# Optimization experiments

Hardware: AMD Instinct MI355X
Metric: run time of the kernel (lower is better)

## Reference

```python
import jax, jax.numpy as jnp
import numpy as np

N = 50000       # num vertices
E_SEG = 80000   # num hyperedges
NNZ = 400000    # incidence pairs
FIN = 512       # input feature dim
H = 256         # MLP_hidden
C = 40          # num classes
NLAYER = 2      # All_num_layers
ALPHA = 0.5     # restart_alpha


def _w(k, shape):
    return jax.random.normal(k, shape, jnp.float32) * (1.0 / np.sqrt(shape[0]))


def setup_inputs() -> dict:
    key = jax.random.key(0)
    ks = jax.random.split(key, 12)
    return {
        "x": jax.random.normal(ks[0], (N, FIN), jnp.float32),
        "vertex": jax.random.randint(ks[1], (NNZ,), 0, N),
        "edges": jax.random.randint(ks[2], (NNZ,), 0, E_SEG),
        "lin_in_w": _w(ks[3], (FIN, H)), "lin_in_b": jnp.zeros((H,), jnp.float32),
        "w1": _w(ks[4], (H, H)),   "b1": jnp.zeros((H,), jnp.float32),
        "w2": _w(ks[5], (2 * H, H)), "b2": jnp.zeros((H,), jnp.float32),
        "w3": _w(ks[6], (H, H)),   "b3": jnp.zeros((H,), jnp.float32),
        "cls_w1": _w(ks[7], (H, H)), "cls_b1": jnp.zeros((H,), jnp.float32),
        "cls_w2": _w(ks[8], (H, C)), "cls_b2": jnp.zeros((C,), jnp.float32),
    }


def reference(x, vertex, edges, lin_in_w, lin_in_b, w1, b1, w2, b2, w3, b3,
              cls_w1, cls_b1, cls_w2, cls_b2):
    # input projection (dropout is identity at p=0)
    x = jax.nn.relu(x @ lin_in_w + lin_in_b)           # [N, H]
    x0 = x
    for _ in range(NLAYER):  # same conv weights reused each layer
        # W1 (1-layer MLP = Linear), gather to incidences
        xve = (x @ w1 + b1)[vertex]                    # [NNZ, H]
        # scatter-add to hyperedges
        xe = jax.ops.segment_sum(xve, edges, num_segments=E_SEG)  # [E, H]
        # gather back, concat with vertex feats, W2 (Linear on 2H)
        xev = jnp.concatenate([x[vertex], xe[edges]], axis=-1) @ w2 + b2  # [NNZ, H]
        # scatter-add to vertices
        xv = jax.ops.segment_sum(xev, vertex, num_segments=N)     # [N, H]
        # restart connection + W (Linear) + outer activation
        x = (1.0 - ALPHA) * xv + ALPHA * x0
        x = jax.nn.relu(x @ w3 + b3)
    # classifier MLP (2 layers: Linear -> relu -> Linear)
    h = jax.nn.relu(x @ cls_w1 + cls_b1)
    return h @ cls_w2 + cls_b2                          # [N, C]
```

## Files before the change

### kernel.cpp

```cpp
#include <hip/hip_runtime.h>
#include <hip/hip_bf16.h>
#include <cstdint>
#include <cstddef>

#define HD   256
#define NV   50000
#define NE   80000
#define NNZC 400000
#define FINC 512
#define NCLS 40

using bf16 = __hip_bfloat16;

typedef short bf16x8v __attribute__((ext_vector_type(8)));
typedef float f32x4   __attribute__((ext_vector_type(4)));
typedef unsigned short u16x8 __attribute__((ext_vector_type(8)));

#define NCH_E ((NE + 1023) / 1024)
#define NCH_V ((NV + 1023) / 1024)
#define NBM_V ((NV + 127) / 128)

__device__ __forceinline__ float b2f(unsigned short u) {
    union { unsigned int i; float f; } c; c.i = ((unsigned int)u) << 16; return c.f;
}
__device__ __forceinline__ unsigned short f2b(float f) {
    union { float f; unsigned int i; } c; c.f = f;
    return (unsigned short)((c.i + 0x7FFFu + ((c.i >> 16) & 1u)) >> 16);
}
__device__ __forceinline__ float4 load4f(const bf16* p) {
    ushort4 u = *reinterpret_cast<const ushort4*>(p);
    return make_float4(b2f(u.x), b2f(u.y), b2f(u.z), b2f(u.w));
}
__device__ __forceinline__ void store4(bf16* p, float4 v) {
    ushort4 u; u.x = f2b(v.x); u.y = f2b(v.y); u.z = f2b(v.z); u.w = f2b(v.w);
    *reinterpret_cast<ushort4*>(p) = u;
}

__device__ __forceinline__ void gl_lds16(const bf16* g, short* l) {
    __builtin_amdgcn_global_load_lds(
        (const __attribute__((address_space(1))) unsigned int*)g,
        (__attribute__((address_space(3))) unsigned int*)l,
        16, 0, 0);
}

__global__ __launch_bounds__(256)
void fill_prep_k(unsigned int* __restrict__ fillp, long long filln,
                 const float* __restrict__ lin_w, const float* __restrict__ w1,
                 const float* __restrict__ w2, const float* __restrict__ w3,
                 const float* __restrict__ cw1, const float* __restrict__ cw2,
                 const float* __restrict__ b2,
                 unsigned short* __restrict__ lin_wt, unsigned short* __restrict__ w1_nb,
                 unsigned short* __restrict__ w2a_nb, unsigned short* __restrict__ w2b_nb,
                 unsigned short* __restrict__ w3t, unsigned short* __restrict__ cw1t,
                 unsigned short* __restrict__ cw2t, float* __restrict__ b2w3)
{
    if (blockIdx.x < 128) {
        long long i = (long long)blockIdx.x * 256 + threadIdx.x;
        for (; i < filln; i += 128 * 256) fillp[i] = 0u;
        return;
    }
    int idx = (blockIdx.x - 128) * 256 + threadIdx.x;
    if (idx < 131072) { int n = idx >> 9, k = idx & 511; lin_wt[idx] = f2b(lin_w[k * 256 + n]); return; }
    idx -= 131072;
    if (idx < 65536) { w1_nb[idx] = f2b(w1[idx]); return; }
    idx -= 65536;
    if (idx < 65536) { w2a_nb[idx] = f2b(w2[idx]); return; }
    idx -= 65536;
    if (idx < 65536) { w2b_nb[idx] = f2b(w2[65536 + idx]); return; }
    idx -= 65536;
    if (idx < 65536) { int n = idx >> 8, k = idx & 255; w3t[idx] = f2b(w3[k * 256 + n]); return; }
    idx -= 65536;
    if (idx < 65536) { int n = idx >> 8, k = idx & 255; cw1t[idx] = f2b(cw1[k * 256 + n]); return; }
    idx -= 65536;
    if (idx < 12288) { int n = idx >> 8, k = idx & 255; cw2t[idx] = f2b((n < NCLS) ? cw2[k * NCLS + n] : 0.f); return; }
    idx -= 12288;
    if (idx < 256) {
        float s = 0.f;
        for (int k = 0; k < 256; ++k) s += b2[k] * w3[k * 256 + idx];
        b2w3[idx] = s;
    }
}

__global__ __launch_bounds__(256)
void hist_k(const int* __restrict__ vertex, const int* __restrict__ edges,
            int* __restrict__ cnt_v, int* __restrict__ cnt_e, int nnz)
{
    int i = blockIdx.x * 256 + threadIdx.x;
    if (i < nnz) {
        atomicAdd(&cnt_v[vertex[i]], 1);
        atomicAdd(&cnt_e[edges[i]], 1);
    }
}

__global__ __launch_bounds__(256)
void scan_part2_k(const int* __restrict__ cnt_e, int* __restrict__ off_e, int* __restrict__ part_e,
                  const int* __restrict__ cnt_v, int* __restrict__ off_v, int* __restrict__ part_v)
{
    const int* cnt; int* off; int* part; int n;
    if (blockIdx.y == 0) { cnt = cnt_e; off = off_e; part = part_e; n = NE; }
    else                 { cnt = cnt_v; off = off_v; part = part_v; n = NV; }
    int base = blockIdx.x * 1024;
    if (base >= n) return;
    __shared__ int s[256];
    int idx = base + threadIdx.x * 4;
    int v[4], sum = 0;
    #pragma unroll
    for (int j = 0; j < 4; ++j) { v[j] = (idx + j < n) ? cnt[idx + j] : 0; sum += v[j]; }
    s[threadIdx.x] = sum;
    __syncthreads();
    #pragma unroll
    for (int d = 1; d < 256; d <<= 1) {
        int t = (threadIdx.x >= d) ? s[threadIdx.x - d] : 0;
        __syncthreads();
        s[threadIdx.x] += t;
        __syncthreads();
    }
    int excl = s[threadIdx.x] - sum;
    #pragma unroll
    for (int j = 0; j < 4; ++j) {
        if (idx + j < n) off[idx + j] = excl;
        excl += v[j];
    }
    if (threadIdx.x == 255) part[blockIdx.x] = s[255];
}

__global__ __launch_bounds__(256)
void scan_top2_k(int* __restrict__ part_e, int* __restrict__ end_e,
                 int* __restrict__ part_v, int* __restrict__ end_v)
{
    int* part; int* endp; int nch;
    if (blockIdx.x == 0) { part = part_e; endp = end_e; nch = NCH_E; }
    else                 { part = part_v; endp = end_v; nch = NCH_V; }
    __shared__ int s[256];
    int v = (threadIdx.x < nch) ? part[threadIdx.x] : 0;
    s[threadIdx.x] = v;
    __syncthreads();
    #pragma unroll
    for (int d = 1; d < 256; d <<= 1) {
        int t = (threadIdx.x >= d) ? s[threadIdx.x - d] : 0;
        __syncthreads();
        s[threadIdx.x] += t;
        __syncthreads();
    }
    if (threadIdx.x < nch) part[threadIdx.x] = s[threadIdx.x] - v;
    if (threadIdx.x == 255) *endp = s[255];
}

__global__ __launch_bounds__(256)
void scan_addcur2_k(int* __restrict__ off_e, const int* __restrict__ part_e, int* __restrict__ cur_e,
                    int* __restrict__ off_v, const int* __restrict__ part_v, int* __restrict__ cur_v)
{
    int n; int* off; const int* part; int* cur;
    if (blockIdx.y == 0) { n = NE; off = off_e; part = part_e; cur = cur_e; }
    else                 { n = NV; off = off_v; part = part_v; cur = cur_v; }
    int i = blockIdx.x * 256 + threadIdx.x;
    if (i < n) { int o = off[i] + part[i >> 10]; off[i] = o; cur[i] = o; }
}

__global__ __launch_bounds__(256)
void csr_fill_k(const int* __restrict__ vertex, const int* __restrict__ edges,
                int* __restrict__ cur_e, int* __restrict__ cur_v,
                int* __restrict__ adj_e, int* __restrict__ adj_v, int nnz)
{
    int i = blockIdx.x * 256 + threadIdx.x;
    if (i >= nnz) return;
    int v = vertex[i], e = edges[i];
    adj_e[atomicAdd(&cur_e[e], 1)] = v;
    adj_v[atomicAdd(&cur_v[v], 1)] = e;
}

__global__ __launch_bounds__(256)
void dege2_k(const int* __restrict__ cnt_e, const int* __restrict__ adj_v,
             const int* __restrict__ off_v, int* __restrict__ dege2, int n)
{
    int v = blockIdx.x * 256 + threadIdx.x;
    if (v >= n) return;
    int s = 0;
    for (int j = off_v[v]; j < off_v[v + 1]; ++j) s += cnt_e[adj_v[j]];
    dege2[v] = s;
}

__global__ __launch_bounds__(256)
void b1w23_k(const float* __restrict__ b1, const unsigned short* __restrict__ W23bt,
             float* __restrict__ o)
{
    int n = threadIdx.x;
    float s = 0.f;
    for (int k = 0; k < 256; ++k) s += b1[k] * b2f(W23bt[n * 256 + k]);
    o[n] = s;
}

template<int EPI, bool AF32>
__global__ __launch_bounds__(256)
void mgemm_k(const void* __restrict__ Agv, const bf16* __restrict__ Bt,
             const float* __restrict__ bias, const float* __restrict__ bias2,
             const int* __restrict__ deg, const int* __restrict__ dege2,
             const bf16* __restrict__ Sb, const bf16* __restrict__ z0b,
             const float* __restrict__ b2w3v, const float* __restrict__ b1w23v,
             bf16* __restrict__ Cg, bf16* __restrict__ Cg2, bf16* __restrict__ Cg3,
             int M, int K, int Nc)
{
    const int nbn = Nc >> 7;
    const int nbm = (M + 127) >> 7;
    const int p   = blockIdx.x;
    const int xcd = p & 7;
    const int q   = p >> 3;
    const int cblk = q % nbn;
    const int rblk = q / nbn;
    const int rb   = rblk * 8 + xcd;
    if (rb >= nbm) return;
    const int bn = cblk * 128;
    const int bm = rb * 128;

    __shared__ __align__(16) short As[2][128 * 64];
    __shared__ __align__(16) short Bs[2][128 * 64];

    const int t  = threadIdx.x;
    const int wv = t >> 6, l = t & 63;
    const int wr = wv >> 1, wc = wv & 1;
    const int l15 = l & 15;

    u16x8 sv8[8], zv8[8];
    float bv[4], bw[4], bb1[4];
    if (EPI == 4) {
        const unsigned short* Sp = (const unsigned short*)Sb + ((size_t)(rb * 2 + cblk) * 256 + t) * 64;
        const unsigned short* Zp = (const unsigned short*)z0b + ((size_t)(rb * 2 + cblk) * 256 + t) * 64;
        #pragma unroll
        for (int j = 0; j < 8; ++j) {
            sv8[j] = *reinterpret_cast<const u16x8*>(Sp + j * 8);
            zv8[j] = *reinterpret_cast<const u16x8*>(Zp + j * 8);
        }
        #pragma unroll
        for (int n = 0; n < 4; ++n) {
            int col = bn + wc * 64 + n * 16 + l15;
            bv[n]  = bias[col];
            bw[n]  = b2w3v[col];
            bb1[n] = b1w23v[col];
        }
    }

    f32x4 acc[4][4];
    #pragma unroll
    for (int m = 0; m < 4; ++m)
        #pragma unroll
        for (int n = 0; n < 4; ++n)
            acc[m][n] = (f32x4){0.f, 0.f, 0.f, 0.f};

    const int brow8   = l >> 3;
    const int bcol_sw = (((l & 7) ^ (l >> 3)) * 8);

    auto stage = [&](int buf, int k0) {
        if constexpr (AF32) {
            const float* Af = (const float*)Agv;
            #pragma unroll
            for (int pi = 0; pi < 4; ++pi) {
                int idx8 = pi * 256 + t;
                int row  = idx8 >> 3;
                int cg   = (idx8 & 7) * 8;
                int ga = bm + row; if (ga >= M) ga = M - 1;
                const float* src = Af + (size_t)ga * K + k0 + cg;
                f32x4 u = *reinterpret_cast<const f32x4*>(src);
                f32x4 v = *reinterpret_cast<const f32x4*>(src + 4);
                bf16x8v o;
                o[0] = (short)f2b(u[0]); o[1] = (short)f2b(u[1]);
                o[2] = (short)f2b(u[2]); o[3] = (short)f2b(u[3]);
                o[4] = (short)f2b(v[0]); o[5] = (short)f2b(v[1]);
                o[6] = (short)f2b(v[2]); o[7] = (short)f2b(v[3]);
                *reinterpret_cast<bf16x8v*>(&As[buf][row * 64 + (cg ^ ((row & 7) * 8))]) = o;
            }
        } else {
            const bf16* Ab = (const bf16*)Agv;
            #pragma unroll
            for (int i = 0; i < 4; ++i) {
                int c = wv * 4 + i;
                int row = c * 8 + brow8;
                int ga = bm + row; if (ga >= M) ga = M - 1;
                gl_lds16(Ab + (size_t)ga * K + k0 + bcol_sw, &As[buf][c * 512]);
            }
        }
        #pragma unroll
        for (int i = 0; i < 4; ++i) {
            int c = wv * 4 + i;
            int row = c * 8 + brow8;
            gl_lds16(Bt + (size_t)(bn + row) * K + k0 + bcol_sw, &Bs[buf][c * 512]);
        }
    };

    stage(0, 0);
    __syncthreads();
    const int nk = K >> 6;
    for (int kst = 0; kst < nk; ++kst) {
        int curb = kst & 1;
        if (kst + 1 < nk) stage(curb ^ 1, (kst + 1) * 64);
        #pragma unroll
        for (int ks = 0; ks < 2; ++ks) {
            bf16x8v a[4], b[4];
            const int kb = ks * 64 + (l >> 4) * 16;
            #pragma unroll
            for (int m = 0; m < 4; ++m) {
                int r = wr * 64 + m * 16 + l15;
                a[m] = *reinterpret_cast<const bf16x8v*>(
                           (const char*)&As[curb][0] + r * 128 + (kb ^ ((r & 7) << 4)));
            }
            #pragma unroll
            for (int n = 0; n < 4; ++n) {
                int r = wc * 64 + n * 16 + l15;
                b[n] = *reinterpret_cast<const bf16x8v*>(
                           (const char*)&Bs[curb][0] + r * 128 + (kb ^ ((r & 7) << 4)));
            }
            #pragma unroll
            for (int m = 0; m < 4; ++m)
                #pragma unroll
                for (int n = 0; n < 4; ++n)
                    acc[m][n] = __builtin_amdgcn_mfma_f32_16x16x32_bf16(a[m], b[n], acc[m][n], 0, 0, 0);
        }
        __syncthreads();
    }

    if (EPI == 5) {
        int oi = bn >> 8;
        bf16* CC = (oi == 0) ? Cg : Cg2;
        int c2 = (bn >> 7) & 1;
        unsigned short* P = (unsigned short*)CC + ((size_t)(rb * 2 + c2) * 256 + t) * 64;
        #pragma unroll
        for (int m = 0; m < 4; ++m) {
            u16x8 o0, o1;
            #pragma unroll
            for (int n = 0; n < 2; ++n)
                #pragma unroll
                for (int i = 0; i < 4; ++i) {
                    o0[n * 4 + i] = f2b(acc[m][n][i]);
                    o1[n * 4 + i] = f2b(acc[m][n + 2][i]);
                }
            *reinterpret_cast<u16x8*>(P + m * 16)     = o0;
            *reinterpret_cast<u16x8*>(P + m * 16 + 8) = o1;
        }
    } else if (EPI == 4) {
        #pragma unroll
        for (int m = 0; m < 4; ++m) {
            #pragma unroll
            for (int i = 0; i < 4; ++i) {
                int row = bm + wr * 64 + m * 16 + (l >> 4) * 4 + i;
                if (row >= M) continue;
                float d   = (float)deg[row];
                float de2 = (float)dege2[row];
                size_t base = (size_t)row * Nc + bn + wc * 64 + l15;
                #pragma unroll
                for (int n = 0; n < 4; ++n) {
                    int e = m * 16 + n * 4 + i;
                    float sv = b2f(sv8[e >> 3][e & 7]);
                    float zv = b2f(zv8[e >> 3][e & 7]);
                    float v = 0.5f * (d * (sv + bw[n]) + acc[m][n][i] + de2 * bb1[n])
                              + 0.5f * zv + bv[n];
                    v = fmaxf(v, 0.f);
                    reinterpret_cast<unsigned short*>(Cg)[base + (size_t)n * 16] = f2b(v);
                }
            }
        }
    } else if (EPI == 3) {
        int oi = bn >> 8;
        bf16* CC = (oi == 0) ? Cg : (oi == 1) ? Cg2 : Cg3;
        const float* bb = (oi == 0) ? bias : (oi == 1) ? bias2 : nullptr;
        int cb = bn & 255;
        float bvv[4];
        #pragma unroll
        for (int n = 0; n < 4; ++n)
            bvv[n] = bb ? bb[cb + wc * 64 + n * 16 + l15] : 0.f;
        #pragma unroll
        for (int m = 0; m < 4; ++m) {
            #pragma unroll
            for (int i = 0; i < 4; ++i) {
                int row = bm + wr * 64 + m * 16 + (l >> 4) * 4 + i;
                if (row >= M) continue;
                size_t base = (size_t)row * 256 + cb + wc * 64 + l15;
                #pragma unroll
                for (int n = 0; n < 4; ++n)
                    reinterpret_cast<unsigned short*>(CC)[base + n * 16] = f2b(acc[m][n][i] + bvv[n]);
            }
        }
    } else {
        float bvv[4];
        #pragma unroll
        for (int n = 0; n < 4; ++n)
            bvv[n] = bias ? bias[bn + wc * 64 + n * 16 + l15] : 0.f;
        #pragma unroll
        for (int m = 0; m < 4; ++m) {
            #pragma unroll
            for (int i = 0; i < 4; ++i) {
                int row = bm + wr * 64 + m * 16 + (l >> 4) * 4 + i;
                if (row >= M) continue;
                size_t base = (size_t)row * Nc + bn + wc * 64 + l15;
                #pragma unroll
                for (int n = 0; n < 4; ++n) {
                    float v = acc[m][n][i] + bvv[n];
                    if (EPI == 1) v = fmaxf(v, 0.f);
                    reinterpret_cast<unsigned short*>(Cg)[base + n * 16] = f2b(v);
                }
            }
        }
    }
}

__global__ __launch_bounds__(256)
void gather_sum_k(const bf16* __restrict__ src, const int* __restrict__ adj,
                  const int* __restrict__ off, bf16* __restrict__ dst, int nseg)
{
    int seg = blockIdx.x * 4 + (threadIdx.x >> 6);
    if (seg >= nseg) return;
    int lane = threadIdx.x & 63;
    int s0 = off[seg], s1 = off[seg + 1];
    float4 acc = make_float4(0.f, 0.f, 0.f, 0.f);
    int j = s0;
    for (; j + 4 <= s1; j += 4) {
        int r0 = adj[j], r1 = adj[j + 1], r2 = adj[j + 2], r3 = adj[j + 3];
        float4 v0 = load4f(src + (size_t)r0 * HD + lane * 4);
        float4 v1 = load4f(src + (size_t)r1 * HD + lane * 4);
        float4 v2 = load4f(src + (size_t)r2 * HD + lane * 4);
        float4 v3 = load4f(src + (size_t)r3 * HD + lane * 4);
        acc.x += (v0.x + v1.x) + (v2.x + v3.x);
        acc.y += (v0.y + v1.y) + (v2.y + v3.y);
        acc.z += (v0.z + v1.z) + (v2.z + v3.z);
        acc.w += (v0.w + v1.w) + (v2.w + v3.w);
    }
    for (; j < s1; ++j) {
        float4 v = load4f(src + (size_t)adj[j] * HD + lane * 4);
        acc.x += v.x; acc.y += v.y; acc.z += v.z; acc.w += v.w;
    }
    store4(dst + (size_t)seg * HD + lane * 4, acc);
}

__global__ __launch_bounds__(256)
void cls_mfma_k(const bf16* __restrict__ Hm, const bf16* __restrict__ Wt,
                const float* __restrict__ bias, float* __restrict__ out, int M)
{
    const int wv = threadIdx.x >> 6, l = threadIdx.x & 63;
    const int l15 = l & 15;
    const int r0 = blockIdx.x * 64 + wv * 16;
    f32x4 acc[3];
    #pragma unroll
    for (int n = 0; n < 3; ++n) acc[n] = (f32x4){0.f, 0.f, 0.f, 0.f};

    int arow = r0 + l15; if (arow >= M) arow = M - 1;
    const int ko = (l >> 4) * 8;
    for (int kk = 0; kk < HD; kk += 32) {
        bf16x8v a = *reinterpret_cast<const bf16x8v*>(Hm + (size_t)arow * HD + kk + ko);
        #pragma unroll
        for (int n = 0; n < 3; ++n) {
            bf16x8v b = *reinterpret_cast<const bf16x8v*>(Wt + (size_t)(n * 16 + l15) * HD + kk + ko);
            acc[n] = __builtin_amdgcn_mfma_f32_16x16x32_bf16(a, b, acc[n], 0, 0, 0);
        }
    }
    #pragma unroll
    for (int n = 0; n < 3; ++n) {
        int col = n * 16 + l15;
        if (col >= NCLS) continue;
        float bv = bias[col];
        #pragma unroll
        for (int i = 0; i < 4; ++i) {
            int row = r0 + (l >> 4) * 4 + i;
            if (row < M) out[(size_t)row * NCLS + col] = acc[n][i] + bv;
        }
    }
}

static inline int xcd_grid(int M, int Nc)
{
    int nbm = (M + 127) >> 7;
    int nbn = Nc >> 7;
    return nbn * (((nbm + 7) / 8) * 8);
}

extern "C" void kernel_launch(void* const* d_in, const int* in_sizes, int n_in,
                              void* d_out, int out_size, void* d_ws, size_t ws_size,
                              hipStream_t stream)
{
    const float* x_in   = (const float*)d_in[0];
    const int*   vertex = (const int*)d_in[1];
    const int*   edges  = (const int*)d_in[2];
    const float* lin_w  = (const float*)d_in[3];
    const float* lin_b  = (const float*)d_in[4];
    const float* w1     = (const float*)d_in[5];
    const float* b1     = (const float*)d_in[6];
    const float* w2     = (const float*)d_in[7];
    const float* b2     = (const float*)d_in[8];
    const float* w3     = (const float*)d_in[9];
    const float* b3     = (const float*)d_in[10];
    const float* cw1    = (const float*)d_in[11];
    const float* cb1    = (const float*)d_in[12];
    const float* cw2    = (const float*)d_in[13];
    const float* cb2    = (const float*)d_in[14];
    float* out = (float*)d_out;
    (void)in_sizes; (void)n_in; (void)out_size; (void)ws_size;

    char* ws = (char*)d_ws;
    const size_t nvhd = (size_t)NV * HD, nehd = (size_t)NE * HD;
    const size_t permsz = (size_t)(NBM_V + 1) * 2 * 256 * 64;
    size_t off = 0;
    auto alloc = [&](size_t bytes) { char* p = ws + off; off += (bytes + 255) & ~(size_t)255; return p; };
    bf16* x0 = (bf16*)alloc(nvhd * 2);
    bf16* xA = (bf16*)alloc(nvhd * 2);
    bf16* E1 = (bf16*)alloc(nehd * 2);
    bf16* E2 = (bf16*)alloc(nehd * 2);
    bf16* S  = (bf16*)alloc(permsz * 2);
    bf16* z0 = (bf16*)alloc(permsz * 2);
    unsigned short* W23at  = (unsigned short*)alloc(2 * 256 * 256 * 2);
    unsigned short* w3t    = W23at + 65536;
    unsigned short* W23bt  = (unsigned short*)alloc(256 * 256 * 2);
    unsigned short* W123bt = (unsigned short*)alloc(256 * 256 * 2);
    unsigned short* w2ab   = (unsigned short*)alloc(512 * 256 * 2);
    unsigned short* w2a_nb = w2ab;
    unsigned short* w2b_nb = w2ab + 256 * 256;
    unsigned short* w1_nb  = (unsigned short*)alloc(256 * 256 * 2);
    unsigned short* lin_wt = (unsigned short*)alloc(256 * 512 * 2);
    unsigned short* cw1t   = (unsigned short*)alloc(256 * 256 * 2);
    unsigned short* cw2t   = (unsigned short*)alloc(48 * 256 * 2);
    float* b2w3  = (float*)alloc(256 * 4);
    float* b1w23 = (float*)alloc(256 * 4);
    int* cnt_e = (int*)alloc(NE * 4);
    int* cnt_v = (int*)alloc(NV * 4);
    int* dege2 = (int*)alloc(NV * 4);
    int* off_e = (int*)alloc((NE + 1) * 4);
    int* off_v = (int*)alloc((NV + 1) * 4);
    int* cur_e = (int*)alloc(NE * 4);
    int* cur_v = (int*)alloc(NV * 4);
    int* part_e = (int*)alloc(256 * 4);
    int* part_v = (int*)alloc(256 * 4);
    int* adj_e = (int*)alloc((size_t)NNZC * 4);
    int* adj_v = (int*)alloc((size_t)NNZC * 4);

    dim3 blk(256);

    fill_prep_k<<<128 + 1841, blk, 0, stream>>>((unsigned int*)cnt_e, NE + NV,
        lin_w, w1, w2, w3, cw1, cw2, b2,
        lin_wt, w1_nb, w2a_nb, w2b_nb, w3t, cw1t, cw2t, b2w3);
    hist_k<<<(NNZC + 255) / 256, blk, 0, stream>>>(vertex, edges, cnt_v, cnt_e, NNZC);
    scan_part2_k<<<dim3(NCH_E, 2), blk, 0, stream>>>(cnt_e, off_e, part_e, cnt_v, off_v, part_v);
    scan_top2_k<<<2, blk, 0, stream>>>(part_e, off_e + NE, part_v, off_v + NV);
    scan_addcur2_k<<<dim3((NE + 255) / 256, 2), blk, 0, stream>>>(off_e, part_e, cur_e,
                                                                  off_v, part_v, cur_v);
    csr_fill_k<<<(NNZC + 255) / 256, blk, 0, stream>>>(vertex, edges, cur_e, cur_v, adj_e, adj_v, NNZC);
    dege2_k<<<(NV + 255) / 256, blk, 0, stream>>>(cnt_e, adj_v, off_v, dege2, NV);

    mgemm_k<3, false><<<xcd_grid(256, 512), blk, 0, stream>>>((const bf16*)w3t, (const bf16*)w2ab,
        nullptr, nullptr, nullptr, nullptr, nullptr, nullptr, nullptr, nullptr,
        (bf16*)W23at, (bf16*)W23bt, nullptr, 256, 256, 512);
    mgemm_k<0, false><<<xcd_grid(256, 256), blk, 0, stream>>>((const bf16*)W23bt, (const bf16*)w1_nb,
        nullptr, nullptr, nullptr, nullptr, nullptr, nullptr, nullptr, nullptr,
        (bf16*)W123bt, nullptr, nullptr, 256, 256, 256);
    b1w23_k<<<1, blk, 0, stream>>>(b1, W23bt, b1w23);

    mgemm_k<1, true><<<xcd_grid(NV, 256), blk, 0, stream>>>(x_in, (const bf16*)lin_wt,
        lin_b, nullptr, nullptr, nullptr, nullptr, nullptr, nullptr, nullptr,
        x0, nullptr, nullptr, NV, FINC, HD);

    const bf16* cur = x0;
    for (int layer = 0; layer < 2; ++layer) {
        if (layer == 0) {
            mgemm_k<5, false><<<xcd_grid(NV, 512), blk, 0, stream>>>(cur, (const bf16*)W23at,
                nullptr, nullptr, nullptr, nullptr, nullptr, nullptr, nullptr, nullptr,
                S, z0, nullptr, NV, HD, 512);
        } else {
            mgemm_k<5, false><<<xcd_grid(NV, 256), blk, 0, stream>>>(cur, (const bf16*)W23at,
                nullptr, nullptr, nullptr, nullptr, nullptr, nullptr, nullptr, nullptr,
                S, nullptr, nullptr, NV, HD, HD);
        }
        gather_sum_k<<<(NE + 3) / 4, blk, 0, stream>>>(cur, adj_e, off_e, E2, NE);
        gather_sum_k<<<(NV + 3) / 4, blk, 0, stream>>>(E2, adj_v, off_v, E1, NV);
        mgemm_k<4, false><<<xcd_grid(NV, 256), blk, 0, stream>>>(E1, (const bf16*)W123bt,
            b3, nullptr, cnt_v, dege2, S, z0, b2w3, b1w23,
            xA, nullptr, nullptr, NV, HD, HD);
        cur = xA;
    }

    mgemm_k<1, false><<<xcd_grid(NV, 256), blk, 0, stream>>>(xA, (const bf16*)cw1t,
        cb1, nullptr, nullptr, nullptr, nullptr, nullptr, nullptr, nullptr,
        E1, nullptr, nullptr, NV, HD, HD);
    cls_mfma_k<<<(NV + 63) / 64, blk, 0, stream>>>(E1, (const bf16*)cw2t, cb2, out, NV);
}
```

Measured before the change: 481.2 us.

## Load A fragments directly from global, stage full 256-wide B slab in LDS

The GEMM kernel stops staging A tiles through double-buffered LDS. Each lane now reads its A fragments straight from global memory, converting from fp32 when needed, while B is loaded into LDS as a whole 128x256 slab once per 256-wide K chunk. This drops the A shared-memory round trip and most per-step barriers. In exchange, A reads are uncoalesced, redundant across the two column waves, and no longer overlap with compute. The larger 64KB B buffer may also reduce occupancy.

```diff
diff --git a/kernel.cpp b/kernel.cpp
--- a/kernel.cpp
+++ b/kernel.cpp
@@ -212,8 +212,7 @@
     const int bn = cblk * 128;
     const int bm = rb * 128;
 
-    __shared__ __align__(16) short As[2][128 * 64];
-    __shared__ __align__(16) short Bs[2][128 * 64];
+    __shared__ __align__(16) short Bs[128 * 256];
 
     const int t  = threadIdx.x;
     const int wv = t >> 6, l = t & 63;
@@ -248,65 +247,60 @@
 
     const int brow8   = l >> 3;
     const int bcol_sw = (((l & 7) ^ (l >> 3)) * 8);
-
-    auto stage = [&](int buf, int k0) {
-        if constexpr (AF32) {
-            const float* Af = (const float*)Agv;
-            #pragma unroll
-            for (int pi = 0; pi < 4; ++pi) {
-                int idx8 = pi * 256 + t;
-                int row  = idx8 >> 3;
-                int cg   = (idx8 & 7) * 8;
-                int ga = bm + row; if (ga >= M) ga = M - 1;
-                const float* src = Af + (size_t)ga * K + k0 + cg;
-                f32x4 u = *reinterpret_cast<const f32x4*>(src);
-                f32x4 v = *reinterpret_cast<const f32x4*>(src + 4);
-                bf16x8v o;
-                o[0] = (short)f2b(u[0]); o[1] = (short)f2b(u[1]);
-                o[2] = (short)f2b(u[2]); o[3] = (short)f2b(u[3]);
-                o[4] = (short)f2b(v[0]); o[5] = (short)f2b(v[1]);
-                o[6] = (short)f2b(v[2]); o[7] = (short)f2b(v[3]);
-                *reinterpret_cast<bf16x8v*>(&As[buf][row * 64 + (cg ^ ((row & 7) * 8))]) = o;
-            }
-        } else {
-            const bf16* Ab = (const bf16*)Agv;
+    const int ko8     = (l >> 4) * 8;
+
+    size_t arow[4];
+    #pragma unroll
+    for (int m = 0; m < 4; ++m) {
+        int ga = bm + wr * 64 + m * 16 + l15; if (ga >= M) ga = M - 1;
+        arow[m] = (size_t)ga * K;
+    }
+
+    for (int kh = 0; kh < K; kh += 256) {
+        if (kh > 0) __syncthreads();
+        #pragma unroll
+        for (int s = 0; s < 4; ++s) {
             #pragma unroll
             for (int i = 0; i < 4; ++i) {
                 int c = wv * 4 + i;
                 int row = c * 8 + brow8;
-                int ga = bm + row; if (ga >= M) ga = M - 1;
-                gl_lds16(Ab + (size_t)ga * K + k0 + bcol_sw, &As[buf][c * 512]);
+                gl_lds16(Bt + (size_t)(bn + row) * K + kh + s * 64 + bcol_sw,
+                         Bs + s * 8192 + c * 512);
             }
         }
-        #pragma unroll
-        for (int i = 0; i < 4; ++i) {
-            int c = wv * 4 + i;
-            int row = c * 8 + brow8;
-            gl_lds16(Bt + (size_t)(bn + row) * K + k0 + bcol_sw, &Bs[buf][c * 512]);
-        }
-    };
-
-    stage(0, 0);
-    __syncthreads();
-    const int nk = K >> 6;
-    for (int kst = 0; kst < nk; ++kst) {
-        int curb = kst & 1;
-        if (kst + 1 < nk) stage(curb ^ 1, (kst + 1) * 64);
-        #pragma unroll
-        for (int ks = 0; ks < 2; ++ks) {
+        __syncthreads();
+
+        #pragma unroll
+        for (int c32 = 0; c32 < 8; ++c32) {
+            int k_abs = kh + c32 * 32 + ko8;
             bf16x8v a[4], b[4];
-            const int kb = ks * 64 + (l >> 4) * 16;
-            #pragma unroll
-            for (int m = 0; m < 4; ++m) {
-                int r = wr * 64 + m * 16 + l15;
-                a[m] = *reinterpret_cast<const bf16x8v*>(
-                           (const char*)&As[curb][0] + r * 128 + (kb ^ ((r & 7) << 4)));
+            if constexpr (AF32) {
+                const float* Af = (const float*)Agv;
+                #pragma unroll
+                for (int m = 0; m < 4; ++m) {
+                    const float* src = Af + arow[m] + k_abs;
+                    f32x4 u = *reinterpret_cast<const f32x4*>(src);
+                    f32x4 v = *reinterpret_cast<const f32x4*>(src + 4);
+                    bf16x8v o;
+                    o[0] = (short)f2b(u[0]); o[1] = (short)f2b(u[1]);
+                    o[2] = (short)f2b(u[2]); o[3] = (short)f2b(u[3]);
+                    o[4] = (short)f2b(v[0]); o[5] = (short)f2b(v[1]);
+                    o[6] = (short)f2b(v[2]); o[7] = (short)f2b(v[3]);
+                    a[m] = o;
+                }
+            } else {
+                const bf16* Ab = (const bf16*)Agv;
+                #pragma unroll
+                for (int m = 0; m < 4; ++m)
+                    a[m] = *reinterpret_cast<const bf16x8v*>(Ab + arow[m] + k_abs);
             }
+            const int kb = (c32 & 1) * 64 + (l >> 4) * 16;
+            const int sB = c32 >> 1;
             #pragma unroll
             for (int n = 0; n < 4; ++n) {
                 int r = wc * 64 + n * 16 + l15;
                 b[n] = *reinterpret_cast<const bf16x8v*>(
-                           (const char*)&Bs[curb][0] + r * 128 + (kb ^ ((r & 7) << 4)));
+                           (const char*)Bs + sB * 16384 + r * 128 + (kb ^ ((r & 7) << 4)));
             }
             #pragma unroll
             for (int m = 0; m < 4; ++m)
@@ -314,7 +308,6 @@
                 for (int n = 0; n < 4; ++n)
                     acc[m][n] = __builtin_amdgcn_mfma_f32_16x16x32_bf16(a[m], b[n], acc[m][n], 0, 0, 0);
         }
-        __syncthreads();
     }
 
     if (EPI == 5) {
```

Result: slower. 575.1 us (+19.5%).
